# Kernel optimization log

Measured on AMD Instinct MI355X. Metric: run time of the kernel, lower is better.

The kernel has to match this reference:

```python
import jax, jax.numpy as jnp
import numpy as np

N, E = 50000, 800000
DIN, DH, DOUT = 128, 128, 64


def _w(k, fan_in, fan_out):
    return (jax.random.normal(k, (fan_in, fan_out), jnp.float32) / np.sqrt(fan_in)).astype(jnp.float32)


def setup_inputs() -> dict:
    key = jax.random.key(0)
    ks = jax.random.split(key, 12)
    x = jax.random.normal(ks[0], (N, DIN), jnp.float32)
    edge_index = jax.random.randint(ks[1], (2, E), 0, N, dtype=jnp.int64)
    return {
        "x": x,
        "edge_index": edge_index,
        # sage1 block: SAGEConv(DIN->DH) -> relu -> SAGEConv(DH->DH)
        "Ws11": _w(ks[2], DIN, DH), "Wn11": _w(ks[3], DIN, DH), "b11": jnp.zeros((DH,), jnp.float32),
        "Ws12": _w(ks[4], DH, DH),  "Wn12": _w(ks[5], DH, DH),  "b12": jnp.zeros((DH,), jnp.float32),
        # sage2 block: SAGEConv(DH->DH) -> relu -> SAGEConv(DH->DH)
        "Ws21": _w(ks[6], DH, DH),  "Wn21": _w(ks[7], DH, DH),  "b21": jnp.zeros((DH,), jnp.float32),
        "Ws22": _w(ks[8], DH, DH),  "Wn22": _w(ks[9], DH, DH),  "b22": jnp.zeros((DH,), jnp.float32),
        # classifier
        "Wc": _w(ks[10], DH, DOUT), "bc": jnp.zeros((DOUT,), jnp.float32),
    }


def _sage_conv(h, src, tgt, Ws, Wn, b, n):
    # mean-aggregate neighbor features (src -> tgt), then self + neighbor linear
    msgs = h[src]                                                   # [E, d] gather
    deg = jax.ops.segment_sum(jnp.ones((src.shape[0],), h.dtype), tgt, num_segments=n)
    agg = jax.ops.segment_sum(msgs, tgt, num_segments=n)
    agg = agg / jnp.maximum(deg, 1.0)[:, None]                      # [n, d]
    return h @ Ws + agg @ Wn + b


def reference(x, edge_index, Ws11, Wn11, b11, Ws12, Wn12, b12,
              Ws21, Wn21, b21, Ws22, Wn22, b22, Wc, bc):
    src, tgt = edge_index[0], edge_index[1]
    n = x.shape[0]
    # sage1 block (2 layers) + outer relu
    h = jax.nn.relu(_sage_conv(x, src, tgt, Ws11, Wn11, b11, n))
    h = _sage_conv(h, src, tgt, Ws12, Wn12, b12, n)
    h = jax.nn.relu(h)
    # dropout (eval mode): identity
    # sage2 block (2 layers) + outer relu
    h = jax.nn.relu(_sage_conv(h, src, tgt, Ws21, Wn21, b21, n))
    h = _sage_conv(h, src, tgt, Ws22, Wn22, b22, n)
    h = jax.nn.relu(h)
    # global mean pool over nodes, then classify
    g = jnp.mean(h, axis=0)                                         # [DH]
    return g @ Wc + bc                                              # [DOUT]
```

## Files before the change

### kernel.cpp

```cpp
#include <hip/hip_runtime.h>
#include <hip/hip_bf16.h>
#include <hip/hip_fp16.h>


typedef _Float16 f16x8 __attribute__((ext_vector_type(8)));
typedef float f32x4 __attribute__((ext_vector_type(4)));

__global__ __launch_bounds__(256) void k_bucket(
    const int* __restrict__ src, const int* __restrict__ tgt,
    int* __restrict__ deg, unsigned long long* __restrict__ staging,
    int* __restrict__ bucket_fill, int E, int bdiv, int cap) {
  __shared__ unsigned long long buf[8][512];
  __shared__ int cnt[8];
  __shared__ int base[8];
  int tid = threadIdx.x;
  if (tid < 8) cnt[tid] = 0;
  __syncthreads();
  int e0 = blockIdx.x * 2048;
#pragma unroll
  for (int i = 0; i < 8; ++i) {
    int e = e0 + i * 256 + tid;
    if (e < E) {
      int t = tgt[e];
      int s = src[e];
      atomicAdd(&deg[t], 1);
      int b = t / bdiv;
      unsigned long long pair =
          ((unsigned long long)(unsigned)t << 32) | (unsigned)s;
      int p = atomicAdd(&cnt[b], 1);
      if (p < 512) {
        buf[b][p] = pair;
      } else {
        int gp = atomicAdd(&bucket_fill[b], 1);
        staging[(size_t)b * cap + gp] = pair;
      }
    }
  }
  __syncthreads();
  if (tid < 8) {
    int c = min(cnt[tid], 512);
    base[tid] = atomicAdd(&bucket_fill[tid], c);
    cnt[tid] = c;
  }
  __syncthreads();
  for (int b = 0; b < 8; ++b) {
    int c = cnt[b];
    for (int p = tid; p < c; p += 256)
      staging[(size_t)b * cap + base[b] + p] = buf[b][p];
  }
}

__global__ __launch_bounds__(256) void k_scatter2(
    const unsigned long long* __restrict__ staging,
    const int* __restrict__ bucket_fill, int* __restrict__ cursor,
    int* __restrict__ csr_src, int cap) {
  int b = blockIdx.x & 7;
  int nchunk = gridDim.x >> 3;
  int chunk = blockIdx.x >> 3;
  int n = bucket_fill[b];
  const unsigned long long* sb = staging + (size_t)b * cap;
  for (int i0 = chunk * 2048; i0 < n; i0 += nchunk * 2048) {
#pragma unroll
    for (int t = 0; t < 8; ++t) {
      int i = i0 + t * 256 + (int)threadIdx.x;
      if (i < n) {
        unsigned long long pair = sb[i];
        int tg = (int)(pair >> 32);
        int s = (int)(pair & 0xffffffffu);
        int pos = atomicAdd(&cursor[tg], 1);
        csr_src[pos] = s;
      }
    }
  }
}

__global__ __launch_bounds__(256) void k_scan1(const int* __restrict__ deg,
                                               int* __restrict__ partial,
                                               int* __restrict__ blocksum,
                                               float* __restrict__ inv_deg, int n) {
  __shared__ int s[256];
  int tid = threadIdx.x;
  int i = blockIdx.x * 256 + tid;
  int v = (i < n) ? deg[i] : 0;
  s[tid] = v;
  __syncthreads();
  for (int off = 1; off < 256; off <<= 1) {
    int t = (tid >= off) ? s[tid - off] : 0;
    __syncthreads();
    s[tid] += t;
    __syncthreads();
  }
  if (i < n) {
    partial[i] = s[tid] - v;
    inv_deg[i] = 1.0f / fmaxf((float)v, 1.0f);
  }
  if (tid == 255) blocksum[blockIdx.x] = s[255];
}

__global__ __launch_bounds__(256) void k_scan2(int* __restrict__ blocksum, int nb) {
  __shared__ int s[256];
  int tid = threadIdx.x;
  int v = (tid < nb) ? blocksum[tid] : 0;
  s[tid] = v;
  __syncthreads();
  for (int off = 1; off < 256; off <<= 1) {
    int t = (tid >= off) ? s[tid - off] : 0;
    __syncthreads();
    s[tid] += t;
    __syncthreads();
  }
  if (tid < nb) blocksum[tid] = s[tid] - v;
}

__global__ __launch_bounds__(256) void k_scan3(const int* __restrict__ partial,
                                               const int* __restrict__ blocksum,
                                               int* __restrict__ row_start,
                                               int* __restrict__ cursor, int n, int E) {
  int i = blockIdx.x * 256 + threadIdx.x;
  if (i < n) {
    int r = partial[i] + blocksum[blockIdx.x];
    row_start[i] = r;
    cursor[i] = r;
  }
  if (i == 0) row_start[n] = E;
}

__global__ __launch_bounds__(256) void k_cvt_x(const float* __restrict__ x,
                                               __half* __restrict__ xh, int total8) {
  int i = blockIdx.x * 256 + threadIdx.x;
  if (i >= total8) return;
  const float4* p = (const float4*)(x + (size_t)i * 8);
  float4 v0 = p[0], v1 = p[1];
  f16x8 o;
  o[0] = (_Float16)v0.x; o[1] = (_Float16)v0.y; o[2] = (_Float16)v0.z; o[3] = (_Float16)v0.w;
  o[4] = (_Float16)v1.x; o[5] = (_Float16)v1.y; o[6] = (_Float16)v1.z; o[7] = (_Float16)v1.w;
  *(f16x8*)(xh + (size_t)i * 8) = o;
}

struct WPack {
  const float* s[4];
  const float* n[4];
};

__global__ __launch_bounds__(256) void k_prep_w(WPack p, __half* __restrict__ Wt) {
  int l = blockIdx.y;
  int i = blockIdx.x * 256 + threadIdx.x;
  int n = i >> 8;
  int k = i & 255;
  const float* W = (k < 128) ? p.s[l] : p.n[l];
  float v = W[(size_t)(k & 127) * 128 + n];
  Wt[(size_t)l * 32768 + (size_t)n * 256 + k] = __float2half(v);
}

__global__ __launch_bounds__(256) void k_agg_h(
    const __half* __restrict__ h, const int* __restrict__ csr_src,
    const int* __restrict__ row_start, const float* __restrict__ inv_deg,
    __half* __restrict__ agg, int n_nodes) {
  int gw = (blockIdx.x * 256 + (int)threadIdx.x) >> 6;
  int lane = threadIdx.x & 63;
  if (gw >= n_nodes) return;
  int q = lane >> 4;
  int dl = (lane & 15) * 8;
  int beg = row_start[gw];
  int end = row_start[gw + 1];
  float a0 = 0.f, a1 = 0.f, a2 = 0.f, a3 = 0.f;
  float a4 = 0.f, a5 = 0.f, a6 = 0.f, a7 = 0.f;
  int e = beg;
  for (; e + 16 <= end; e += 16) {
    int i0 = csr_src[e + q];
    int i1 = csr_src[e + 4 + q];
    int i2 = csr_src[e + 8 + q];
    int i3 = csr_src[e + 12 + q];
    f16x8 v0 = *(const f16x8*)(h + (size_t)i0 * 128 + dl);
    f16x8 v1 = *(const f16x8*)(h + (size_t)i1 * 128 + dl);
    f16x8 v2 = *(const f16x8*)(h + (size_t)i2 * 128 + dl);
    f16x8 v3 = *(const f16x8*)(h + (size_t)i3 * 128 + dl);
    a0 += ((float)v0[0] + (float)v1[0]) + ((float)v2[0] + (float)v3[0]);
    a1 += ((float)v0[1] + (float)v1[1]) + ((float)v2[1] + (float)v3[1]);
    a2 += ((float)v0[2] + (float)v1[2]) + ((float)v2[2] + (float)v3[2]);
    a3 += ((float)v0[3] + (float)v1[3]) + ((float)v2[3] + (float)v3[3]);
    a4 += ((float)v0[4] + (float)v1[4]) + ((float)v2[4] + (float)v3[4]);
    a5 += ((float)v0[5] + (float)v1[5]) + ((float)v2[5] + (float)v3[5]);
    a6 += ((float)v0[6] + (float)v1[6]) + ((float)v2[6] + (float)v3[6]);
    a7 += ((float)v0[7] + (float)v1[7]) + ((float)v2[7] + (float)v3[7]);
  }
  for (; e + 8 <= end; e += 8) {
    int i0 = csr_src[e + q];
    int i1 = csr_src[e + 4 + q];
    f16x8 v0 = *(const f16x8*)(h + (size_t)i0 * 128 + dl);
    f16x8 v1 = *(const f16x8*)(h + (size_t)i1 * 128 + dl);
    a0 += (float)v0[0] + (float)v1[0];
    a1 += (float)v0[1] + (float)v1[1];
    a2 += (float)v0[2] + (float)v1[2];
    a3 += (float)v0[3] + (float)v1[3];
    a4 += (float)v0[4] + (float)v1[4];
    a5 += (float)v0[5] + (float)v1[5];
    a6 += (float)v0[6] + (float)v1[6];
    a7 += (float)v0[7] + (float)v1[7];
  }
  for (; e + 4 <= end; e += 4) {
    int i0 = csr_src[e + q];
    f16x8 v0 = *(const f16x8*)(h + (size_t)i0 * 128 + dl);
    a0 += (float)v0[0];
    a1 += (float)v0[1];
    a2 += (float)v0[2];
    a3 += (float)v0[3];
    a4 += (float)v0[4];
    a5 += (float)v0[5];
    a6 += (float)v0[6];
    a7 += (float)v0[7];
  }
  if (e + q < end) {
    int i0 = csr_src[e + q];
    f16x8 v0 = *(const f16x8*)(h + (size_t)i0 * 128 + dl);
    a0 += (float)v0[0];
    a1 += (float)v0[1];
    a2 += (float)v0[2];
    a3 += (float)v0[3];
    a4 += (float)v0[4];
    a5 += (float)v0[5];
    a6 += (float)v0[6];
    a7 += (float)v0[7];
  }
  a0 += __shfl_xor(a0, 16, 64);
  a1 += __shfl_xor(a1, 16, 64);
  a2 += __shfl_xor(a2, 16, 64);
  a3 += __shfl_xor(a3, 16, 64);
  a4 += __shfl_xor(a4, 16, 64);
  a5 += __shfl_xor(a5, 16, 64);
  a6 += __shfl_xor(a6, 16, 64);
  a7 += __shfl_xor(a7, 16, 64);
  a0 += __shfl_xor(a0, 32, 64);
  a1 += __shfl_xor(a1, 32, 64);
  a2 += __shfl_xor(a2, 32, 64);
  a3 += __shfl_xor(a3, 32, 64);
  a4 += __shfl_xor(a4, 32, 64);
  a5 += __shfl_xor(a5, 32, 64);
  a6 += __shfl_xor(a6, 32, 64);
  a7 += __shfl_xor(a7, 32, 64);
  if (q == 0) {
    float wgt = inv_deg[gw];
    f16x8 r;
    r[0] = (_Float16)(a0 * wgt);
    r[1] = (_Float16)(a1 * wgt);
    r[2] = (_Float16)(a2 * wgt);
    r[3] = (_Float16)(a3 * wgt);
    r[4] = (_Float16)(a4 * wgt);
    r[5] = (_Float16)(a5 * wgt);
    r[6] = (_Float16)(a6 * wgt);
    r[7] = (_Float16)(a7 * wgt);
    *(f16x8*)(agg + (size_t)gw * 128 + dl) = r;
  }
}

__global__ __launch_bounds__(256) void k_linear_mfma(
    const __half* __restrict__ h, const __half* __restrict__ agg,
    const __half* __restrict__ Wt, const float* __restrict__ bias,
    __half* __restrict__ out, int n_nodes) {
  int tid = threadIdx.x;
  int wave = tid >> 6;
  int lane = tid & 63;
  int m0 = blockIdx.x * 64 + wave * 16;
  int lr = lane & 15;
  int lg = lane >> 4;
  f32x4 acc[8];
#pragma unroll
  for (int ct = 0; ct < 8; ++ct) acc[ct] = (f32x4){0.f, 0.f, 0.f, 0.f};

  int arow = m0 + lr;
  if (arow >= n_nodes) arow = n_nodes - 1;
  const __half* hrow = h + (size_t)arow * 128;
  const __half* grow = agg + (size_t)arow * 128;

#pragma unroll
  for (int ks = 0; ks < 8; ++ks) {
    const __half* srcp = (ks < 4) ? hrow : grow;
    int koff = (ks & 3) * 32 + lg * 8;
    f16x8 a = *(const f16x8*)(srcp + koff);
    int kb = ks * 32 + lg * 8;
#pragma unroll
    for (int ct = 0; ct < 8; ++ct) {
      f16x8 b = *(const f16x8*)(Wt + (size_t)(ct * 16 + lr) * 256 + kb);
      acc[ct] = __builtin_amdgcn_mfma_f32_16x16x32_f16(a, b, acc[ct], 0, 0, 0);
    }
  }

#pragma unroll
  for (int ct = 0; ct < 8; ++ct) {
    int n_col = ct * 16 + lr;
    float bv = bias[n_col];
#pragma unroll
    for (int r = 0; r < 4; ++r) {
      int m = m0 + lg * 4 + r;
      if (m < n_nodes)
        out[(size_t)m * 128 + n_col] = __float2half(fmaxf(acc[ct][r] + bv, 0.f));
    }
  }
}

__global__ __launch_bounds__(256) void k_pool(const __half* __restrict__ h,
                                              float* __restrict__ partial, int n_nodes) {
  __shared__ float red[4][128];
  int tid = threadIdx.x;
  int lane = tid & 63;
  int w = tid >> 6;
  float a0 = 0.f, a1 = 0.f;
  for (int n = blockIdx.x * 4 + w; n < n_nodes; n += gridDim.x * 4) {
    float2 f = __half22float2(*(const __half2*)(h + (size_t)n * 128 + lane * 2));
    a0 += f.x;
    a1 += f.y;
  }
  red[w][lane * 2] = a0;
  red[w][lane * 2 + 1] = a1;
  __syncthreads();
  if (tid < 128) {
    partial[(size_t)blockIdx.x * 128 + tid] =
        (red[0][tid] + red[1][tid]) + (red[2][tid] + red[3][tid]);
  }
}

__global__ __launch_bounds__(512) void k_final(const float* __restrict__ partial,
                                               const float* __restrict__ Wc,
                                               const float* __restrict__ bc,
                                               float* __restrict__ out, int n_nodes) {
  __shared__ float red[4][128];
  __shared__ float gs[128];
  __shared__ float red2[8][64];
  int tid = threadIdx.x;
  int j = tid & 127;
  int c = tid >> 7;
  float s = 0.f;
#pragma unroll
  for (int b = 0; b < 64; ++b) s += partial[(size_t)(c * 64 + b) * 128 + j];
  red[c][j] = s;
  __syncthreads();
  if (tid < 128) {
    float g = (red[0][tid] + red[1][tid]) + (red[2][tid] + red[3][tid]);
    gs[tid] = g / (float)n_nodes;
  }
  __syncthreads();
  {
    int jo = tid & 63;
    int c2 = tid >> 6;
    float s2 = 0.f;
#pragma unroll
    for (int d = 0; d < 16; ++d)
      s2 += gs[c2 * 16 + d] * Wc[(size_t)(c2 * 16 + d) * 64 + jo];
    red2[c2][jo] = s2;
  }
  __syncthreads();
  if (tid < 64) {
    float o = bc[tid];
#pragma unroll
    for (int c2 = 0; c2 < 8; ++c2) o += red2[c2][tid];
    out[tid] = o;
  }
}

extern "C" void kernel_launch(void* const* d_in, const int* in_sizes, int n_in,
                              void* d_out, int out_size, void* d_ws, size_t ws_size,
                              hipStream_t stream) {
  const float* x = (const float*)d_in[0];
  const int* ei = (const int*)d_in[1];
  const float* Ws11 = (const float*)d_in[2];
  const float* Wn11 = (const float*)d_in[3];
  const float* b11 = (const float*)d_in[4];
  const float* Ws12 = (const float*)d_in[5];
  const float* Wn12 = (const float*)d_in[6];
  const float* b12 = (const float*)d_in[7];
  const float* Ws21 = (const float*)d_in[8];
  const float* Wn21 = (const float*)d_in[9];
  const float* b21 = (const float*)d_in[10];
  const float* Ws22 = (const float*)d_in[11];
  const float* Wn22 = (const float*)d_in[12];
  const float* b22 = (const float*)d_in[13];
  const float* Wc = (const float*)d_in[14];
  const float* bc = (const float*)d_in[15];

  int N = in_sizes[0] / 128;
  int E = in_sizes[1] / 2;
  const int* src = ei;
  const int* tgt = ei + E;

  int bdiv = (N + 7) / 8;
  int cap = E / 8 + 8192;

  char* w = (char*)d_ws;
  size_t off = 0;
  auto alloc = [&](size_t bytes) {
    void* p = w + off;
    off += (bytes + 255) & ~(size_t)255;
    return p;
  };
  __half* xh = (__half*)alloc((size_t)N * 128 * 2);
  __half* hA = (__half*)alloc((size_t)N * 128 * 2);
  __half* hB = (__half*)alloc((size_t)N * 128 * 2);
  __half* aggb = (__half*)alloc((size_t)N * 128 * 2);
  __half* Wt = (__half*)alloc((size_t)4 * 32768 * 2);
  float* partial = (float*)alloc((size_t)256 * 128 * 4);
  float* inv_deg = (float*)alloc((size_t)N * 4);
  int* deg = (int*)alloc((size_t)N * 4);
  int* row_start = (int*)alloc((size_t)(N + 1) * 4);
  int* cursor = (int*)alloc((size_t)N * 4);
  int* csr_src = (int*)alloc((size_t)E * 4);
  int* scanp = (int*)alloc((size_t)N * 4);
  int* blocksum = (int*)alloc((size_t)256 * 4);
  unsigned long long* staging =
      (unsigned long long*)alloc((size_t)8 * cap * 8);
  int* bucket_fill = (int*)alloc((size_t)8 * 4);

  hipMemsetAsync(deg, 0, (size_t)N * 4, stream);
  hipMemsetAsync(bucket_fill, 0, 8 * 4, stream);
  hipMemsetAsync(partial, 0, (size_t)256 * 128 * 4, stream);

  int nb = (N + 255) / 256;
  int bb = (E + 2047) / 2048;
  k_bucket<<<bb, 256, 0, stream>>>(src, tgt, deg, staging, bucket_fill, E, bdiv, cap);
  k_scan1<<<nb, 256, 0, stream>>>(deg, scanp, blocksum, inv_deg, N);
  k_scan2<<<1, 256, 0, stream>>>(blocksum, nb);
  k_scan3<<<nb, 256, 0, stream>>>(scanp, blocksum, row_start, cursor, N, E);
  k_scatter2<<<448, 256, 0, stream>>>(staging, bucket_fill, cursor, csr_src, cap);

  int total8 = N * 128 / 8;
  k_cvt_x<<<(total8 + 255) / 256, 256, 0, stream>>>(x, xh, total8);
  WPack wp;
  wp.s[0] = Ws11; wp.s[1] = Ws12; wp.s[2] = Ws21; wp.s[3] = Ws22;
  wp.n[0] = Wn11; wp.n[1] = Wn12; wp.n[2] = Wn21; wp.n[3] = Wn22;
  k_prep_w<<<dim3(128, 4), 256, 0, stream>>>(wp, Wt);

  int ab = (N + 3) / 4;
  int lb = (N + 63) / 64;

  k_agg_h<<<ab, 256, 0, stream>>>(xh, csr_src, row_start, inv_deg, aggb, N);
  k_linear_mfma<<<lb, 256, 0, stream>>>(xh, aggb, Wt + 0 * 32768, b11, hA, N);
  k_agg_h<<<ab, 256, 0, stream>>>(hA, csr_src, row_start, inv_deg, aggb, N);
  k_linear_mfma<<<lb, 256, 0, stream>>>(hA, aggb, Wt + 1 * 32768, b12, hB, N);
  k_agg_h<<<ab, 256, 0, stream>>>(hB, csr_src, row_start, inv_deg, aggb, N);
  k_linear_mfma<<<lb, 256, 0, stream>>>(hB, aggb, Wt + 2 * 32768, b21, hA, N);
  k_agg_h<<<ab, 256, 0, stream>>>(hA, csr_src, row_start, inv_deg, aggb, N);
  k_linear_mfma<<<lb, 256, 0, stream>>>(hA, aggb, Wt + 3 * 32768, b22, hB, N);

  k_pool<<<256, 256, 0, stream>>>(hB, partial, N);
  k_final<<<1, 512, 0, stream>>>(partial, Wc, bc, (float*)d_out, N);
}
```

Baseline: 389.2 us.

## Aggregate bucket-slot atomics per wave and split linear tile by column quarters

The bucketing kernel now uses a wave ballot per bucket, so one leader lane does a single LDS atomicAdd per bucket and the other lanes take offsets from a prefix popcount. The per-bucket shared buffer shrinks from 512 to 320 entries, which lowers LDS use but sends more edges to the global overflow path. In the MFMA linear kernel each wave now computes all 64 rows for a 32-column slice instead of 16 rows for all 128 columns. This cuts per-wave weight loads, but each A row is loaded by all four waves.

```diff
diff --git a/kernel.cpp b/kernel.cpp
--- a/kernel.cpp
+++ b/kernel.cpp
@@ -10,35 +10,51 @@
     const int* __restrict__ src, const int* __restrict__ tgt,
     int* __restrict__ deg, unsigned long long* __restrict__ staging,
     int* __restrict__ bucket_fill, int E, int bdiv, int cap) {
-  __shared__ unsigned long long buf[8][512];
+  __shared__ unsigned long long buf[8][320];
   __shared__ int cnt[8];
   __shared__ int base[8];
   int tid = threadIdx.x;
+  int lane = tid & 63;
   if (tid < 8) cnt[tid] = 0;
   __syncthreads();
   int e0 = blockIdx.x * 2048;
 #pragma unroll
   for (int i = 0; i < 8; ++i) {
     int e = e0 + i * 256 + tid;
-    if (e < E) {
+    bool valid = e < E;
+    int b = -1;
+    unsigned long long pair = 0;
+    if (valid) {
       int t = tgt[e];
       int s = src[e];
       atomicAdd(&deg[t], 1);
-      int b = t / bdiv;
-      unsigned long long pair =
-          ((unsigned long long)(unsigned)t << 32) | (unsigned)s;
-      int p = atomicAdd(&cnt[b], 1);
-      if (p < 512) {
-        buf[b][p] = pair;
-      } else {
-        int gp = atomicAdd(&bucket_fill[b], 1);
-        staging[(size_t)b * cap + gp] = pair;
+      b = t / bdiv;
+      pair = ((unsigned long long)(unsigned)t << 32) | (unsigned)s;
+    }
+#pragma unroll
+    for (int bk = 0; bk < 8; ++bk) {
+      bool mine = (b == bk);
+      unsigned long long mask = __ballot(mine);
+      if (mask == 0ull) continue;
+      int cw = __popcll(mask);
+      int leader = __ffsll((unsigned long long)mask) - 1;
+      int p0 = 0;
+      if (lane == leader) p0 = atomicAdd(&cnt[bk], cw);
+      p0 = __shfl(p0, leader, 64);
+      if (mine) {
+        int p = p0 + __popcll(mask & ((1ull << lane) - 1ull));
+        if (p < 320) {
+          buf[bk][p] = pair;
+        } else {
+          int gp = atomicAdd(&bucket_fill[bk], 1);
+          staging[(size_t)bk * cap + gp] = pair;
+        }
       }
     }
   }
   __syncthreads();
   if (tid < 8) {
-    int c = min(cnt[tid], 512);
+    int c = min(cnt[tid], 320);
     base[tid] = atomicAdd(&bucket_fill[tid], c);
     cnt[tid] = c;
   }
@@ -258,42 +274,55 @@
     const __half* __restrict__ Wt, const float* __restrict__ bias,
     __half* __restrict__ out, int n_nodes) {
   int tid = threadIdx.x;
-  int wave = tid >> 6;
+  int cq = tid >> 6;
   int lane = tid & 63;
-  int m0 = blockIdx.x * 64 + wave * 16;
+  int node0 = blockIdx.x * 64;
   int lr = lane & 15;
   int lg = lane >> 4;
-  f32x4 acc[8];
-#pragma unroll
-  for (int ct = 0; ct < 8; ++ct) acc[ct] = (f32x4){0.f, 0.f, 0.f, 0.f};
-
-  int arow = m0 + lr;
-  if (arow >= n_nodes) arow = n_nodes - 1;
-  const __half* hrow = h + (size_t)arow * 128;
-  const __half* grow = agg + (size_t)arow * 128;
+
+  f32x4 acc[4][2];
+#pragma unroll
+  for (int rt = 0; rt < 4; ++rt)
+#pragma unroll
+    for (int ct = 0; ct < 2; ++ct) acc[rt][ct] = (f32x4){0.f, 0.f, 0.f, 0.f};
+
+  const __half* hrow[4];
+  const __half* grow[4];
+#pragma unroll
+  for (int rt = 0; rt < 4; ++rt) {
+    int arow = node0 + rt * 16 + lr;
+    if (arow >= n_nodes) arow = n_nodes - 1;
+    hrow[rt] = h + (size_t)arow * 128;
+    grow[rt] = agg + (size_t)arow * 128;
+  }
 
 #pragma unroll
   for (int ks = 0; ks < 8; ++ks) {
-    const __half* srcp = (ks < 4) ? hrow : grow;
     int koff = (ks & 3) * 32 + lg * 8;
-    f16x8 a = *(const f16x8*)(srcp + koff);
     int kb = ks * 32 + lg * 8;
-#pragma unroll
-    for (int ct = 0; ct < 8; ++ct) {
-      f16x8 b = *(const f16x8*)(Wt + (size_t)(ct * 16 + lr) * 256 + kb);
-      acc[ct] = __builtin_amdgcn_mfma_f32_16x16x32_f16(a, b, acc[ct], 0, 0, 0);
+    f16x8 b0 = *(const f16x8*)(Wt + (size_t)(cq * 32 + lr) * 256 + kb);
+    f16x8 b1 = *(const f16x8*)(Wt + (size_t)(cq * 32 + 16 + lr) * 256 + kb);
+#pragma unroll
+    for (int rt = 0; rt < 4; ++rt) {
+      f16x8 a = (ks < 4) ? *(const f16x8*)(hrow[rt] + koff)
+                         : *(const f16x8*)(grow[rt] + koff);
+      acc[rt][0] = __builtin_amdgcn_mfma_f32_16x16x32_f16(a, b0, acc[rt][0], 0, 0, 0);
+      acc[rt][1] = __builtin_amdgcn_mfma_f32_16x16x32_f16(a, b1, acc[rt][1], 0, 0, 0);
     }
   }
 
 #pragma unroll
-  for (int ct = 0; ct < 8; ++ct) {
-    int n_col = ct * 16 + lr;
+  for (int ct = 0; ct < 2; ++ct) {
+    int n_col = cq * 32 + ct * 16 + lr;
     float bv = bias[n_col];
 #pragma unroll
-    for (int r = 0; r < 4; ++r) {
-      int m = m0 + lg * 4 + r;
-      if (m < n_nodes)
-        out[(size_t)m * 128 + n_col] = __float2half(fmaxf(acc[ct][r] + bv, 0.f));
+    for (int rt = 0; rt < 4; ++rt) {
+#pragma unroll
+      for (int r = 0; r < 4; ++r) {
+        int m = node0 + rt * 16 + lg * 4 + r;
+        if (m < n_nodes)
+          out[(size_t)m * 128 + n_col] = __float2half(fmaxf(acc[rt][ct][r] + bv, 0.f));
+      }
     }
   }
 }
```

After: 348.4 us. -10.5%, faster.
